# Performance work log

Measured on AMD Instinct MI355X. Metric: run time of the kernel, lower is better.

The kernel has to match this reference:

```python
import jax, jax.numpy as jnp
import numpy as np
import math

B, P, PIX, D, C = 128, 256, 256, 512, 10
MAX_STEPS, TOL, EPS = 4, 1e-3, 1e-5


def setup_inputs() -> dict:
    key = jax.random.key(0)
    ks = jax.random.split(key, 12)
    pi = math.pi
    return {
        "x": jax.random.normal(ks[0], (B, P, PIX), jnp.float32),
        "Wp": jax.random.normal(ks[1], (D, PIX), jnp.float32) * (1.0 / math.sqrt(PIX)),
        "bp": jnp.zeros((D,), jnp.float32),
        "q_rot": jax.random.uniform(ks[2], (D,), jnp.float32, -pi, pi),
        "k_rot": jax.random.uniform(ks[3], (D,), jnp.float32, -pi, pi),
        "v_rot": jax.random.uniform(ks[4], (D,), jnp.float32, -pi, pi),
        "ff_real": jax.random.normal(ks[5], (D, D), jnp.float32) * (1.0 / math.sqrt(D)),
        "ff_imag": jax.random.uniform(ks[6], (D, D), jnp.float32, -0.01, 0.01),
        "Wr": jax.random.normal(ks[7], (C, D), jnp.float32) * 0.05,
        "br": jnp.zeros((C,), jnp.float32),
        "Wi": jax.random.normal(ks[8], (C, D), jnp.float32) * 0.05,
        "bi": jnp.zeros((C,), jnp.float32),
    }


def _complex_norm(x):
    # normalize magnitude stats over last dim, preserve phase (torch.std uses ddof=1)
    mag = jnp.abs(x)
    mean_mag = jnp.mean(mag, axis=-1, keepdims=True)
    std_mag = jnp.std(mag, axis=-1, keepdims=True, ddof=1)
    norm_mag = (mag - mean_mag) / (std_mag + EPS)
    scale = jnp.tanh(norm_mag) / (mag + EPS)
    return x * scale


def _fro(z):
    return jnp.sqrt(jnp.sum(jnp.abs(z) ** 2))


def _pos_phase():
    pos = jnp.arange(P, dtype=jnp.float32)[:, None]
    dim = jnp.arange(D, dtype=jnp.float32)[None, :]
    freq = 1.0 / (10000.0 ** (dim / D))
    return pos * freq * math.pi  # (P, D)


def reference(x, Wp, bp, q_rot, k_rot, v_rot, ff_real, ff_imag, Wr, br, Wi, bi):
    mag = jnp.tanh(jnp.einsum('bpi,di->bpd', x, Wp) + bp)
    state = mag.astype(jnp.complex64) * jnp.exp(1j * _pos_phase())[None]  # (B,P,D)
    ff = (ff_real + 1j * ff_imag).astype(jnp.complex64)
    eq, ek, ev = jnp.exp(1j * q_rot), jnp.exp(1j * k_rot), jnp.exp(1j * v_rot)
    scale = 8.0 / math.sqrt(D)
    active = jnp.array(True)
    for _ in range(MAX_STEPS):  # fixed small iteration count; updates frozen after convergence
        prev = state
        q, k, v = state * eq, state * ek, state * ev
        interference = jnp.einsum('bpd,bqd->bpq', q, jnp.conj(k))
        attn = jax.nn.softmax(interference.real * scale, axis=-1)
        attn_out = jnp.einsum('bpq,bqd->bpd', attn.astype(jnp.complex64), v)
        new_state = _complex_norm((prev + attn_out) @ ff)
        diff = _fro(new_state - prev) / (_fro(new_state) + 1e-8)
        state = jnp.where(active, new_state, prev)
        active = jnp.logical_and(active, diff >= TOL)
    pooled = jnp.mean(state, axis=1)  # (B,D) complex
    logits = pooled.real @ Wr.T + br + pooled.imag @ Wi.T + bi
    return logits
```

## Files before the change

kernel.cpp:

```cpp
#include <hip/hip_runtime.h>
#include <math.h>

#define BB   128
#define PP   256
#define PIX_ 256
#define DD   512
#define CC   10
#define MTOT (BB*PP)
#define NK   1024
#define KA   2048
#define KB2  2048
#define NSLOT (MTOT/4)

static constexpr float SCALE_F = 0.35355339059327373f;
static constexpr float PI_F    = 3.14159265358979323846f;

typedef short bf16x8 __attribute__((ext_vector_type(8)));
typedef float f32x4  __attribute__((ext_vector_type(4)));
typedef unsigned short ushort8 __attribute__((ext_vector_type(8)));

__device__ __forceinline__ unsigned short f2bf(float f) {
    union { float f; unsigned u; } v; v.f = f;
    unsigned r = v.u + 0x7FFF + ((v.u >> 16) & 1);
    return (unsigned short)(r >> 16);
}
__device__ __forceinline__ float bf2f(unsigned short h) {
    union { unsigned u; float f; } v; v.u = ((unsigned)h) << 16;
    return v.f;
}

typedef __attribute__((address_space(3))) unsigned lds_u32;
typedef __attribute__((address_space(1))) const unsigned glb_u32;
__device__ __forceinline__ void gl2lds16(const unsigned short* g, short* l) {
    __builtin_amdgcn_global_load_lds((glb_u32*)g, (lds_u32*)l, 16, 0, 0);
}

__global__ void k_setup(const float* __restrict__ q_rot, const float* __restrict__ k_rot,
                        const float* __restrict__ v_rot,
                        float* __restrict__ freq, float* __restrict__ cd, float* __restrict__ sd,
                        float* __restrict__ cv, float* __restrict__ sv,
                        int* __restrict__ active) {
    int t = threadIdx.x;
    if (t < DD) {
        freq[t] = expf(-(float)t * (9.210340371976184f / 512.0f));
        float dl = q_rot[t] - k_rot[t];
        cd[t] = cosf(dl);       sd[t] = sinf(dl);
        cv[t] = cosf(v_rot[t]); sv[t] = sinf(v_rot[t]);
    }
    if (t == 0) *active = 1;
}

__global__ __launch_bounds__(256) void k_tab(const float* __restrict__ freq,
                                             float* __restrict__ Tc, float* __restrict__ Ts) {
    const int p = blockIdx.x, t = threadIdx.x;
#pragma unroll
    for (int j = 0; j < 2; j++) {
        const int d = t * 2 + j;
        float s, c; sincosf((float)p * freq[d] * PI_F, &s, &c);
        Tc[(size_t)p * DD + d] = c;
        Ts[(size_t)p * DD + d] = s;
    }
}

__global__ __launch_bounds__(256) void k_prep2(const float* __restrict__ Fr, const float* __restrict__ Fi,
                                               unsigned short* __restrict__ Bt2) {
    const int n = blockIdx.x;
    const int t = threadIdx.x;
    unsigned short* row = Bt2 + (size_t)n * KB2;
#pragma unroll
    for (int j4 = 0; j4 < 4; j4++) {
        const int j = j4 * 256 + t;
        float v;
        if (n < 512) v = (j < 512) ? Fr[(size_t)j * DD + n] : -Fi[(size_t)(j - 512) * DD + n];
        else         v = (j < 512) ? Fi[(size_t)j * DD + (n - 512)] : Fr[(size_t)(j - 512) * DD + (n - 512)];
        const unsigned short hi = f2bf(v);
        row[j] = hi;
        row[NK + j] = f2bf(v - bf2f(hi));
    }
}

#define SCAT4(TILE, V4) do { TILE[lk+0][lrow]=(V4).x; TILE[lk+1][lrow]=(V4).y; \
                             TILE[lk+2][lrow]=(V4).z; TILE[lk+3][lrow]=(V4).w; } while(0)

__global__ __launch_bounds__(256) void k_init(const float* __restrict__ x,
        const float* __restrict__ Wp, const float* __restrict__ bp,
        const float* __restrict__ Tc, const float* __restrict__ Ts,
        float* __restrict__ Sr, float* __restrict__ Si) {
    __shared__ float As[16][68];
    __shared__ float Bs[16][68];
    const int bm = blockIdx.y * 64, bn = blockIdx.x * 64;
    const int t = threadIdx.x, tx = t & 15, ty = t >> 4;
    const int lrow = t >> 2, lk = (t & 3) * 4;
    float acc[4][4] = {};
    for (int k0 = 0; k0 < PIX_; k0 += 16) {
        const float4 a4 = *(const float4*)(x  + (size_t)(bm + lrow) * PIX_ + k0 + lk);
        const float4 b4 = *(const float4*)(Wp + (size_t)(bn + lrow) * PIX_ + k0 + lk);
        __syncthreads();
        SCAT4(As, a4);
        SCAT4(Bs, b4);
        __syncthreads();
#pragma unroll
        for (int kk = 0; kk < 16; ++kk) {
            const float4 av = *(const float4*)&As[kk][ty * 4];
            const float4 bv = *(const float4*)&Bs[kk][tx * 4];
            const float a[4] = {av.x, av.y, av.z, av.w};
            const float b[4] = {bv.x, bv.y, bv.z, bv.w};
#pragma unroll
            for (int i = 0; i < 4; i++)
#pragma unroll
                for (int j = 0; j < 4; j++) acc[i][j] = fmaf(a[i], b[j], acc[i][j]);
        }
    }
#pragma unroll
    for (int i = 0; i < 4; i++) {
        const int m = bm + ty * 4 + i;
        const int p = m & 255;
        const float4 c4 = *(const float4*)(Tc + (size_t)p * DD + bn + tx * 4);
        const float4 s4 = *(const float4*)(Ts + (size_t)p * DD + bn + tx * 4);
        const float cphv[4] = {c4.x, c4.y, c4.z, c4.w};
        const float sphv[4] = {s4.x, s4.y, s4.z, s4.w};
        float4 vr, vi;
        float* pvr = (float*)&vr; float* pvi = (float*)&vi;
#pragma unroll
        for (int j = 0; j < 4; j++) {
            const int d = bn + tx * 4 + j;
            const float mg = tanhf(acc[i][j] + bp[d]);
            pvr[j] = mg * cphv[j]; pvi[j] = mg * sphv[j];
        }
        *(float4*)(Sr + (size_t)m * DD + bn + tx * 4) = vr;
        *(float4*)(Si + (size_t)m * DD + bn + tx * 4) = vi;
    }
}

__global__ __launch_bounds__(256) void k_xy(const float* __restrict__ Sr, const float* __restrict__ Si,
        const float* __restrict__ cd, const float* __restrict__ sd,
        unsigned short* X, unsigned short* Y,
        const int* __restrict__ active) {
    if (*active == 0) return;
    const int r = blockIdx.x, t = threadIdx.x;
    const size_t base = (size_t)r * DD + 2 * t;
    const float2 s_r = *(const float2*)(Sr + base);
    const float2 s_i = *(const float2*)(Si + base);
    const float2 c2  = *(const float2*)(cd + 2 * t);
    const float2 s2  = *(const float2*)(sd + 2 * t);
    unsigned short* xr = X + (size_t)r * KA;
    unsigned short* yr = Y + (size_t)r * KA;
    const float srv[2] = {s_r.x, s_r.y}, siv[2] = {s_i.x, s_i.y};
    const float cv_[2] = {c2.x, c2.y},  sv_[2] = {s2.x, s2.y};
    ushort2 xh_r, xh_i, xl_r, xl_i, yh_r, yh_i, yl_r, yl_i;
    unsigned short* o[8] = {(unsigned short*)&xh_r, (unsigned short*)&xh_i,
                            (unsigned short*)&xl_r, (unsigned short*)&xl_i,
                            (unsigned short*)&yh_r, (unsigned short*)&yh_i,
                            (unsigned short*)&yl_r, (unsigned short*)&yl_i};
#pragma unroll
    for (int e = 0; e < 2; e++) {
        const unsigned short hr = f2bf(srv[e]);
        const unsigned short hi_ = f2bf(siv[e]);
        o[0][e] = hr;  o[2][e] = f2bf(srv[e] - bf2f(hr));
        o[1][e] = hi_; o[3][e] = f2bf(siv[e] - bf2f(hi_));
        const float krr = srv[e] * cv_[e] + siv[e] * sv_[e];
        const float kri = siv[e] * cv_[e] - srv[e] * sv_[e];
        const unsigned short yh1 = f2bf(krr);
        const unsigned short yh2 = f2bf(kri);
        o[4][e] = yh1; o[6][e] = f2bf(krr - bf2f(yh1));
        o[5][e] = yh2; o[7][e] = f2bf(kri - bf2f(yh2));
    }
    *(ushort2*)(xr + 2 * t)        = xh_r;
    *(ushort2*)(xr + 512 + 2 * t)  = xh_i;
    *(ushort2*)(xr + 1024 + 2 * t) = xl_r;
    *(ushort2*)(xr + 1536 + 2 * t) = xl_i;
    *(ushort2*)(yr + 2 * t)        = yh_r;
    *(ushort2*)(yr + 512 + 2 * t)  = yh_i;
    *(ushort2*)(yr + 1024 + 2 * t) = yl_r;
    *(ushort2*)(yr + 1536 + 2 * t) = yl_i;
}

__global__ __launch_bounds__(256) void k_score_sm(const unsigned short* __restrict__ X,
        const unsigned short* __restrict__ Y,
        unsigned short* __restrict__ Asp, const int* __restrict__ active) {
    if (*active == 0) return;
    __shared__ short SM[20480];
    short* XH = SM;
    short* XL = SM + 2048;
    short* YH = SM + 4096;
    short* YL = SM + 12288;
    const int t = threadIdx.x;
    const int w = t >> 6, L = t & 63;
    const int lane15 = L & 15, quad = L >> 4;
    const int nsm = (int)gridDim.x >> 2;
    const int s   = (int)blockIdx.x & (nsm - 1);
    const int rt  = (int)blockIdx.x / nsm;
    const int bm = s * 256 + rt * 64;
    const int yb = s * 256;
    const int gr = t >> 2, ch = (t & 3) * 8;
    short* XHw = XH + w * 512;
    short* XLw = XL + w * 512;
    short* YHw = YH + w * 512;
    short* YLw = YL + w * 512;
    f32x4 acc[16] = {};
    for (int k0 = 0; k0 < 1024; k0 += 32) {
        __syncthreads();
        gl2lds16(X + (size_t)(bm + gr) * KA + k0 + ch,        XHw);
        gl2lds16(X + (size_t)(bm + gr) * KA + 1024 + k0 + ch, XLw);
#pragma unroll
        for (int ss = 0; ss < 4; ss++) {
            gl2lds16(Y + (size_t)(yb + ss * 64 + gr) * KA + k0 + ch,        YHw + ss * 2048);
            gl2lds16(Y + (size_t)(yb + ss * 64 + gr) * KA + 1024 + k0 + ch, YLw + ss * 2048);
        }
        __syncthreads();
        const bf16x8 xh = *(const bf16x8*)(XH + (w * 16 + lane15) * 32 + quad * 8);
        const bf16x8 xl = *(const bf16x8*)(XL + (w * 16 + lane15) * 32 + quad * 8);
#pragma unroll
        for (int tc = 0; tc < 16; tc++) {
            const bf16x8 yh = *(const bf16x8*)(YH + (tc * 16 + lane15) * 32 + quad * 8);
            acc[tc] = __builtin_amdgcn_mfma_f32_16x16x32_bf16(xh, yh, acc[tc], 0, 0, 0);
            acc[tc] = __builtin_amdgcn_mfma_f32_16x16x32_bf16(xl, yh, acc[tc], 0, 0, 0);
            const bf16x8 yl = *(const bf16x8*)(YL + (tc * 16 + lane15) * 32 + quad * 8);
            acc[tc] = __builtin_amdgcn_mfma_f32_16x16x32_bf16(xh, yl, acc[tc], 0, 0, 0);
        }
    }
#pragma unroll
    for (int tc = 0; tc < 16; tc++) acc[tc] *= SCALE_F;
#pragma unroll
    for (int r = 0; r < 4; r++) {
        float mx = acc[0][r];
#pragma unroll
        for (int tc = 1; tc < 16; tc++) mx = fmaxf(mx, acc[tc][r]);
#pragma unroll
        for (int off = 8; off; off >>= 1) mx = fmaxf(mx, __shfl_xor(mx, off, 64));
        float sum = 0.f;
#pragma unroll
        for (int tc = 0; tc < 16; tc++) { acc[tc][r] = __expf(acc[tc][r] - mx); sum += acc[tc][r]; }
#pragma unroll
        for (int off = 8; off; off >>= 1) sum += __shfl_xor(sum, off, 64);
        const float inv = 1.0f / sum;
#pragma unroll
        for (int tc = 0; tc < 16; tc++) acc[tc][r] *= inv;
    }
    __syncthreads();
#pragma unroll
    for (int h = 0; h < 2; h++) {
        if ((w >> 1) == h) {
#pragma unroll
            for (int r = 0; r < 4; r++) {
                const int lr = (w & 1) * 16 + quad * 4 + r;
#pragma unroll
                for (int tc = 0; tc < 16; tc++) {
                    const float p = acc[tc][r];
                    const unsigned short hi = f2bf(p);
                    SM[lr * 520 + tc * 16 + lane15] = (short)hi;
                    SM[lr * 520 + 256 + tc * 16 + lane15] = (short)f2bf(p - bf2f(hi));
                }
            }
        }
        __syncthreads();
        unsigned short* dst = Asp + (size_t)(bm + h * 32) * 512;
#pragma unroll
        for (int k = 0; k < 8; k++) {
            const int c = t + 256 * k;
            const int row = c >> 6, off = (c & 63) * 8;
            *(ushort8*)(dst + (size_t)c * 8) = *(const ushort8*)&SM[row * 520 + off];
        }
        __syncthreads();
    }
}

__global__ __launch_bounds__(256) void k_attnout_mfma(const unsigned short* __restrict__ Asp,
        const unsigned short* __restrict__ X,
        const float* __restrict__ Sr, const float* __restrict__ Si,
        const float* __restrict__ cv, const float* __restrict__ sv,
        unsigned short* __restrict__ A2, const int* __restrict__ active) {
    if (*active == 0) return;
    __shared__ short AhT[128][32];
    __shared__ short AlT[128][32];
    __shared__ short BH[128][40];
    __shared__ short BL[128][40];
    const int t = threadIdx.x;
    const int w = t >> 6, L = t & 63;
    const int lane15 = L & 15, quad = L >> 4;
    const int bm = blockIdx.x * 128;
    const int bn = blockIdx.y * 64;
    const int sample = blockIdx.x >> 1;
    const int gr = t >> 2, ch = (t & 3) * 8;
    short* AhW0 = &AhT[0][0] + w * 512;
    short* AhW1 = AhW0 + 64 * 32;
    short* AlW0 = &AlT[0][0] + w * 512;
    short* AlW1 = AlW0 + 64 * 32;
    const int nn = t & 127, kh = t >> 7;
    const unsigned short* Bsrc = X + (size_t)sample * PP * KA
                               + ((nn < 64) ? (bn + nn) : (512 + bn + nn - 64));
    f32x4 acc[2][8] = {};
    for (int q0 = 0; q0 < PP; q0 += 32) {
        __syncthreads();
        gl2lds16(Asp + (size_t)(bm + gr) * 512      + q0 + ch,       AhW0);
        gl2lds16(Asp + (size_t)(bm + 64 + gr) * 512 + q0 + ch,       AhW1);
        gl2lds16(Asp + (size_t)(bm + gr) * 512      + 256 + q0 + ch, AlW0);
        gl2lds16(Asp + (size_t)(bm + 64 + gr) * 512 + 256 + q0 + ch, AlW1);
#pragma unroll
        for (int kg = 0; kg < 2; kg++) {
            const int qb = kh * 16 + kg * 8;
            bf16x8 hh, ll;
#pragma unroll
            for (int j = 0; j < 8; j++) {
                const size_t o = (size_t)(q0 + qb + j) * KA;
                hh[j] = (short)Bsrc[o];
                ll[j] = (short)Bsrc[o + 1024];
            }
            *(bf16x8*)&BH[nn][qb] = hh;
            *(bf16x8*)&BL[nn][qb] = ll;
        }
        __syncthreads();
        bf16x8 bh[8];
#pragma unroll
        for (int tc = 0; tc < 8; tc++)
            bh[tc] = *(const bf16x8*)&BH[tc * 16 + lane15][quad * 8];
        bf16x8 afh[2];
#pragma unroll
        for (int tr = 0; tr < 2; tr++) {
            afh[tr] = *(const bf16x8*)&AhT[w * 32 + tr * 16 + lane15][quad * 8];
            const bf16x8 afl = *(const bf16x8*)&AlT[w * 32 + tr * 16 + lane15][quad * 8];
#pragma unroll
            for (int tc = 0; tc < 8; tc++)
                acc[tr][tc] = __builtin_amdgcn_mfma_f32_16x16x32_bf16(afh[tr], bh[tc], acc[tr][tc], 0, 0, 0);
#pragma unroll
            for (int tc = 0; tc < 8; tc++)
                acc[tr][tc] = __builtin_amdgcn_mfma_f32_16x16x32_bf16(afl, bh[tc], acc[tr][tc], 0, 0, 0);
        }
#pragma unroll
        for (int tc = 0; tc < 8; tc++) {
            const bf16x8 bl = *(const bf16x8*)&BL[tc * 16 + lane15][quad * 8];
            acc[0][tc] = __builtin_amdgcn_mfma_f32_16x16x32_bf16(afh[0], bl, acc[0][tc], 0, 0, 0);
            acc[1][tc] = __builtin_amdgcn_mfma_f32_16x16x32_bf16(afh[1], bl, acc[1][tc], 0, 0, 0);
        }
    }
#pragma unroll
    for (int tr = 0; tr < 2; tr++) {
#pragma unroll
        for (int tc = 0; tc < 4; tc++) {
            const int d = bn + tc * 16 + lane15;
            const float cvd = cv[d], svd = sv[d];
#pragma unroll
            for (int r = 0; r < 4; r++) {
                const int m = bm + w * 32 + tr * 16 + quad * 4 + r;
                const float wr = acc[tr][tc][r];
                const float wi = acc[tr][tc + 4][r];
                const float tr_ = Sr[(size_t)m * DD + d] + (wr * cvd - wi * svd);
                const float ti_ = Si[(size_t)m * DD + d] + (wr * svd + wi * cvd);
                const unsigned short rh = f2bf(tr_);
                const unsigned short ih = f2bf(ti_);
                unsigned short* arow = A2 + (size_t)m * KA;
                arow[d]        = rh;
                arow[512 + d]  = ih;
                arow[1024 + d] = f2bf(tr_ - bf2f(rh));
                arow[1536 + d] = f2bf(ti_ - bf2f(ih));
            }
        }
    }
}

__global__ __launch_bounds__(256) void k_ff_mfma2(const unsigned short* __restrict__ A2,
        const unsigned short* __restrict__ Bt2,
        float* __restrict__ U, const int* __restrict__ active) {
    if (*active == 0) return;
    __shared__ short AH[128][32], AL[128][32];
    __shared__ short BH[128][32], BL[128][32];
    const int t = threadIdx.x;
    const int w = t >> 6, L = t & 63;
    const int lane15 = L & 15, quad = L >> 4;
    const int bm = blockIdx.x * 128, bn = blockIdx.y * 128;
    const int gr = t >> 2, ch = (t & 3) * 8;
    short* AHw = &AH[0][0] + w * 512;
    short* ALw = &AL[0][0] + w * 512;
    short* BHw = &BH[0][0] + w * 512;
    short* BLw = &BL[0][0] + w * 512;
    f32x4 acc[2][8] = {};
    for (int k0 = 0; k0 < 1024; k0 += 32) {
        __syncthreads();
        gl2lds16(A2  + (size_t)(bm + gr) * KA       + k0 + ch,        AHw);
        gl2lds16(A2  + (size_t)(bm + 64 + gr) * KA  + k0 + ch,        AHw + 64 * 32);
        gl2lds16(A2  + (size_t)(bm + gr) * KA       + 1024 + k0 + ch, ALw);
        gl2lds16(A2  + (size_t)(bm + 64 + gr) * KA  + 1024 + k0 + ch, ALw + 64 * 32);
        gl2lds16(Bt2 + (size_t)(bn + gr) * KB2      + k0 + ch,        BHw);
        gl2lds16(Bt2 + (size_t)(bn + 64 + gr) * KB2 + k0 + ch,        BHw + 64 * 32);
        gl2lds16(Bt2 + (size_t)(bn + gr) * KB2      + 1024 + k0 + ch, BLw);
        gl2lds16(Bt2 + (size_t)(bn + 64 + gr) * KB2 + 1024 + k0 + ch, BLw + 64 * 32);
        __syncthreads();
        bf16x8 ah[2], al[2];
#pragma unroll
        for (int tr = 0; tr < 2; tr++) {
            ah[tr] = *(const bf16x8*)&AH[w * 32 + tr * 16 + lane15][quad * 8];
            al[tr] = *(const bf16x8*)&AL[w * 32 + tr * 16 + lane15][quad * 8];
        }
#pragma unroll
        for (int tc = 0; tc < 8; tc++) {
            const bf16x8 bh = *(const bf16x8*)&BH[tc * 16 + lane15][quad * 8];
            acc[0][tc] = __builtin_amdgcn_mfma_f32_16x16x32_bf16(ah[0], bh, acc[0][tc], 0, 0, 0);
            acc[1][tc] = __builtin_amdgcn_mfma_f32_16x16x32_bf16(ah[1], bh, acc[1][tc], 0, 0, 0);
            acc[0][tc] = __builtin_amdgcn_mfma_f32_16x16x32_bf16(al[0], bh, acc[0][tc], 0, 0, 0);
            acc[1][tc] = __builtin_amdgcn_mfma_f32_16x16x32_bf16(al[1], bh, acc[1][tc], 0, 0, 0);
            const bf16x8 bl = *(const bf16x8*)&BL[tc * 16 + lane15][quad * 8];
            acc[0][tc] = __builtin_amdgcn_mfma_f32_16x16x32_bf16(ah[0], bl, acc[0][tc], 0, 0, 0);
            acc[1][tc] = __builtin_amdgcn_mfma_f32_16x16x32_bf16(ah[1], bl, acc[1][tc], 0, 0, 0);
        }
    }
#pragma unroll
    for (int tr = 0; tr < 2; tr++)
#pragma unroll
        for (int tc = 0; tc < 8; tc++) {
            const int n = bn + tc * 16 + lane15;
            const int mbase = bm + w * 32 + tr * 16 + quad * 4;
#pragma unroll
            for (int r = 0; r < 4; r++)
                U[(size_t)(mbase + r) * NK + n] = acc[tr][tc][r];
        }
}

__global__ __launch_bounds__(256) void k_norm(const float* U,
        float* __restrict__ Sr, float* __restrict__ Si,
        float* __restrict__ part,
        unsigned short* X, unsigned short* Y,
        const float* __restrict__ cd, const float* __restrict__ sd,
        const int wxy, const int* __restrict__ active) {
    if (*active == 0) return;
    __shared__ float red[8];
    const int t = threadIdx.x, rt = t >> 6, L = t & 63;
    const int row = blockIdx.x * 4 + rt;
    const size_t ub = (size_t)row * NK;
    const size_t base = (size_t)row * DD;
    const float4 ur0 = *(const float4*)(U + ub + 4 * L);
    const float4 ur1 = *(const float4*)(U + ub + 256 + 4 * L);
    const float4 ui0 = *(const float4*)(U + ub + 512 + 4 * L);
    const float4 ui1 = *(const float4*)(U + ub + 768 + 4 * L);
    const float4 pr0 = *(const float4*)(Sr + base + 4 * L);
    const float4 pr1 = *(const float4*)(Sr + base + 256 + 4 * L);
    const float4 pi0 = *(const float4*)(Si + base + 4 * L);
    const float4 pi1 = *(const float4*)(Si + base + 256 + 4 * L);
    const float urr[8] = {ur0.x, ur0.y, ur0.z, ur0.w, ur1.x, ur1.y, ur1.z, ur1.w};
    const float uii[8] = {ui0.x, ui0.y, ui0.z, ui0.w, ui1.x, ui1.y, ui1.z, ui1.w};
    float mg[8], msum = 0.f;
#pragma unroll
    for (int e = 0; e < 8; e++) {
        mg[e] = sqrtf(urr[e] * urr[e] + uii[e] * uii[e]);
        msum += mg[e];
    }
#pragma unroll
    for (int off = 32; off; off >>= 1) msum += __shfl_xor(msum, off, 64);
    const float mean = msum * (1.0f / 512.0f);
    float vs = 0.f;
#pragma unroll
    for (int e = 0; e < 8; e++) { const float d = mg[e] - mean; vs += d * d; }
#pragma unroll
    for (int off = 32; off; off >>= 1) vs += __shfl_xor(vs, off, 64);
    const float istd = 1.0f / (sqrtf(vs * (1.0f / 511.0f)) + 1e-5f);
    float nr[8], ni[8];
#pragma unroll
    for (int e = 0; e < 8; e++) {
        const float sc = tanhf((mg[e] - mean) * istd) / (mg[e] + 1e-5f);
        nr[e] = urr[e] * sc; ni[e] = uii[e] * sc;
    }
    const float prr[8] = {pr0.x, pr0.y, pr0.z, pr0.w, pr1.x, pr1.y, pr1.z, pr1.w};
    const float pii[8] = {pi0.x, pi0.y, pi0.z, pi0.w, pi1.x, pi1.y, pi1.z, pi1.w};
    float dd = 0.f, nn = 0.f;
#pragma unroll
    for (int e = 0; e < 8; e++) {
        const float dr = nr[e] - prr[e], di = ni[e] - pii[e];
        dd += dr * dr + di * di;
        nn += nr[e] * nr[e] + ni[e] * ni[e];
    }
    *(float4*)(Sr + base + 4 * L)       = make_float4(nr[0], nr[1], nr[2], nr[3]);
    *(float4*)(Sr + base + 256 + 4 * L) = make_float4(nr[4], nr[5], nr[6], nr[7]);
    *(float4*)(Si + base + 4 * L)       = make_float4(ni[0], ni[1], ni[2], ni[3]);
    *(float4*)(Si + base + 256 + 4 * L) = make_float4(ni[4], ni[5], ni[6], ni[7]);
    if (wxy) {
        unsigned short* xr = X + (size_t)row * KA;
        unsigned short* yr = Y + (size_t)row * KA;
        const float4 c0 = *(const float4*)(cd + 4 * L);
        const float4 c1 = *(const float4*)(cd + 256 + 4 * L);
        const float4 s0 = *(const float4*)(sd + 4 * L);
        const float4 s1 = *(const float4*)(sd + 256 + 4 * L);
        const float cdv[8] = {c0.x, c0.y, c0.z, c0.w, c1.x, c1.y, c1.z, c1.w};
        const float sdv[8] = {s0.x, s0.y, s0.z, s0.w, s1.x, s1.y, s1.z, s1.w};
        ushort4 xhr[2], xhi[2], xlr[2], xli[2], yhr[2], yhi[2], ylr[2], yli[2];
#pragma unroll
        for (int e = 0; e < 8; e++) {
            const int g = e >> 2, j = e & 3;
            const unsigned short hr = f2bf(nr[e]);
            const unsigned short hi_ = f2bf(ni[e]);
            ((unsigned short*)&xhr[g])[j] = hr;
            ((unsigned short*)&xlr[g])[j] = f2bf(nr[e] - bf2f(hr));
            ((unsigned short*)&xhi[g])[j] = hi_;
            ((unsigned short*)&xli[g])[j] = f2bf(ni[e] - bf2f(hi_));
            const float krr = nr[e] * cdv[e] + ni[e] * sdv[e];
            const float kri = ni[e] * cdv[e] - nr[e] * sdv[e];
            const unsigned short k1 = f2bf(krr);
            const unsigned short k2 = f2bf(kri);
            ((unsigned short*)&yhr[g])[j] = k1;
            ((unsigned short*)&ylr[g])[j] = f2bf(krr - bf2f(k1));
            ((unsigned short*)&yhi[g])[j] = k2;
            ((unsigned short*)&yli[g])[j] = f2bf(kri - bf2f(k2));
        }
        *(ushort4*)(xr + 4 * L)        = xhr[0]; *(ushort4*)(xr + 256 + 4 * L)  = xhr[1];
        *(ushort4*)(xr + 512 + 4 * L)  = xhi[0]; *(ushort4*)(xr + 768 + 4 * L)  = xhi[1];
        *(ushort4*)(xr + 1024 + 4 * L) = xlr[0]; *(ushort4*)(xr + 1280 + 4 * L) = xlr[1];
        *(ushort4*)(xr + 1536 + 4 * L) = xli[0]; *(ushort4*)(xr + 1792 + 4 * L) = xli[1];
        *(ushort4*)(yr + 4 * L)        = yhr[0]; *(ushort4*)(yr + 256 + 4 * L)  = yhr[1];
        *(ushort4*)(yr + 512 + 4 * L)  = yhi[0]; *(ushort4*)(yr + 768 + 4 * L)  = yhi[1];
        *(ushort4*)(yr + 1024 + 4 * L) = ylr[0]; *(ushort4*)(yr + 1280 + 4 * L) = ylr[1];
        *(ushort4*)(yr + 1536 + 4 * L) = yli[0]; *(ushort4*)(yr + 1792 + 4 * L) = yli[1];
    }
#pragma unroll
    for (int off = 32; off; off >>= 1) {
        dd += __shfl_xor(dd, off, 64);
        nn += __shfl_xor(nn, off, 64);
    }
    if (L == 0) { red[rt] = dd; red[4 + rt] = nn; }
    __syncthreads();
    if (t == 0)
        *(float2*)(part + 2 * blockIdx.x) =
            make_float2(red[0] + red[1] + red[2] + red[3],
                        red[4] + red[5] + red[6] + red[7]);
}

__global__ __launch_bounds__(256) void k_flag(const float* __restrict__ part, int* __restrict__ active) {
    __shared__ float red[8];
    const int t = threadIdx.x, rt = t >> 6, L = t & 63;
    float dd = 0.f, nn = 0.f;
    for (int i = t; i < NSLOT; i += 256) {
        const float2 p = *(const float2*)(part + 2 * i);
        dd += p.x; nn += p.y;
    }
#pragma unroll
    for (int off = 32; off; off >>= 1) {
        dd += __shfl_xor(dd, off, 64);
        nn += __shfl_xor(nn, off, 64);
    }
    if (L == 0) { red[rt] = dd; red[4 + rt] = nn; }
    __syncthreads();
    if (t == 0) {
        const float d = red[0] + red[1] + red[2] + red[3];
        const float n = red[4] + red[5] + red[6] + red[7];
        const float diff = sqrtf(d) / (sqrtf(n) + 1e-8f);
        const int a = *active;
        *active = (a && (diff >= 1e-3f)) ? 1 : 0;
    }
}

__global__ __launch_bounds__(256) void k_pool(const float* __restrict__ Sr, const float* __restrict__ Si,
        float* __restrict__ Pr, float* __restrict__ Pi) {
    const int gid = blockIdx.x * 256 + threadIdx.x;
    const int b = gid >> 9, d = gid & 511;
    const size_t base = (size_t)b * PP * DD + d;
    float sr = 0.f, si = 0.f;
    for (int p = 0; p < PP; p++) {
        sr += Sr[base + (size_t)p * DD];
        si += Si[base + (size_t)p * DD];
    }
    Pr[gid] = sr * (1.0f / 256.0f);
    Pi[gid] = si * (1.0f / 256.0f);
}

__global__ __launch_bounds__(64) void k_logits(const float* __restrict__ Pr, const float* __restrict__ Pi,
        const float* __restrict__ Wr, const float* __restrict__ br,
        const float* __restrict__ Wi, const float* __restrict__ bi,
        float* __restrict__ out) {
    const int b = blockIdx.x;
    const int lane = threadIdx.x;
    for (int c = 0; c < CC; c++) {
        float acc = 0.f;
#pragma unroll
        for (int k = 0; k < 8; k++) {
            const int d = lane + 64 * k;
            acc += Pr[b * DD + d] * Wr[c * DD + d] + Pi[b * DD + d] * Wi[c * DD + d];
        }
#pragma unroll
        for (int off = 32; off; off >>= 1) acc += __shfl_xor(acc, off, 64);
        if (lane == 0) out[b * CC + c] = acc + br[c] + bi[c];
    }
}

extern "C" void kernel_launch(void* const* d_in, const int* in_sizes, int n_in,
                              void* d_out, int out_size, void* d_ws, size_t ws_size,
                              hipStream_t stream) {
    const float* x     = (const float*)d_in[0];
    const float* Wp    = (const float*)d_in[1];
    const float* bp    = (const float*)d_in[2];
    const float* q_rot = (const float*)d_in[3];
    const float* k_rot = (const float*)d_in[4];
    const float* v_rot = (const float*)d_in[5];
    const float* ffr   = (const float*)d_in[6];
    const float* ffi   = (const float*)d_in[7];
    const float* Wr    = (const float*)d_in[8];
    const float* br    = (const float*)d_in[9];
    const float* Wi    = (const float*)d_in[10];
    const float* bi    = (const float*)d_in[11];
    float* out = (float*)d_out;

    float* ws = (float*)d_ws;
    const size_t plane = (size_t)MTOT * DD;
    const size_t sline = (size_t)PP * DD;

    float* freq = ws;
    float* cd   = freq + DD;
    float* sd   = cd + DD;
    float* cv   = sd + DD;
    float* sv   = cv + DD;
    int*   active = (int*)(sv + DD);
    float* Pr = ws + 4096;
    float* Pi = Pr + (size_t)BB * DD;
    float* part = Pi + (size_t)BB * DD;
    float* Sr = part + 2 * NSLOT;
    float* Si = Sr + plane;
    unsigned short* Bt2 = (unsigned short*)(Si + plane);
    float* Tc = (float*)(Bt2 + (size_t)NK * KB2);
    float* Ts = Tc + (size_t)PP * DD;
    float* chunkbase = Si + plane + (size_t)NK * 3072 / 2;

    const size_t fixed_f = (4096 + 2 * (size_t)BB * DD + 2 * NSLOT) + 2 * plane + (size_t)NK * 3072 / 2;
    const size_t perC_f = (size_t)PP * NK * 2 + (size_t)PP * 256;

    int C = BB;
    while (C > 1 && (fixed_f + (size_t)C * perC_f) * 4ull > ws_size) C >>= 1;
    const int fullXY = (C == BB);

    float* U = chunkbase;
    unsigned short* X  = (unsigned short*)chunkbase;
    float* Yf = chunkbase + (size_t)C * PP * NK;
    unsigned short* Y  = (unsigned short*)Yf;
    unsigned short* A2 = Y;
    unsigned short* Asp = (unsigned short*)(Yf + (size_t)C * PP * NK);

    k_setup<<<1, 512, 0, stream>>>(q_rot, k_rot, v_rot, freq, cd, sd, cv, sv, active);
    k_tab<<<PP, 256, 0, stream>>>(freq, Tc, Ts);
    k_prep2<<<NK, 256, 0, stream>>>(ffr, ffi, Bt2);
    k_init<<<dim3(DD / 64, MTOT / 64), 256, 0, stream>>>(x, Wp, bp, Tc, Ts, Sr, Si);

    for (int it = 0; it < 4; ++it) {
        for (int c0 = 0; c0 < BB; c0 += C) {
            float* Sr_c = Sr + (size_t)c0 * sline;
            float* Si_c = Si + (size_t)c0 * sline;
            float* part_c = part + (size_t)c0 * (PP / 4) * 2;
            if (!fullXY || it == 0)
                k_xy<<<C * PP, 256, 0, stream>>>(Sr_c, Si_c, cd, sd, X, Y, active);
            k_score_sm<<<C * 4, 256, 0, stream>>>(X, Y, Asp, active);
            k_attnout_mfma<<<dim3(C * 2, 8), 256, 0, stream>>>(Asp, X, Sr_c, Si_c, cv, sv, A2, active);
            k_ff_mfma2<<<dim3(C * 2, NK / 128), 256, 0, stream>>>(A2, Bt2, U, active);
            k_norm<<<C * (PP / 4), 256, 0, stream>>>(U, Sr_c, Si_c, part_c, X, Y, cd, sd, fullXY, active);
        }
        k_flag<<<1, 256, 0, stream>>>(part, active);
    }

    k_pool<<<BB * DD / 256, 256, 0, stream>>>(Sr, Si, Pr, Pi);
    k_logits<<<BB, 64, 0, stream>>>(Pr, Pi, Wr, br, Wi, bi, out);
}
```

Measured before the change: 3.003 ms.

## Drop fp32 state planes; keep state only as packed hi/lo bf16 X

When the workspace is large enough, the fp32 Sr/Si state planes are removed and the state is carried only as packed hi+lo bf16 in X. k_init writes X and Y directly, so the first k_xy pass is skipped. k_attnout, k_norm and k_pool rebuild fp32 values from hi+lo, which cuts fp32 state reads and writes per iteration. The state is now held to roughly bf16x2 precision instead of full fp32, and the old chunked path stays as a fallback.

```diff
diff --git a/kernel.cpp b/kernel.cpp
--- a/kernel.cpp
+++ b/kernel.cpp
@@ -85,7 +85,10 @@
 __global__ __launch_bounds__(256) void k_init(const float* __restrict__ x,
         const float* __restrict__ Wp, const float* __restrict__ bp,
         const float* __restrict__ Tc, const float* __restrict__ Ts,
-        float* __restrict__ Sr, float* __restrict__ Si) {
+        float* Sr, float* Si,
+        unsigned short* X, unsigned short* Y,
+        const float* __restrict__ cd, const float* __restrict__ sd,
+        const int packed) {
     __shared__ float As[16][68];
     __shared__ float Bs[16][68];
     const int bm = blockIdx.y * 64, bn = blockIdx.x * 64;
@@ -111,6 +114,10 @@
                 for (int j = 0; j < 4; j++) acc[i][j] = fmaf(a[i], b[j], acc[i][j]);
         }
     }
+    const float4 cd4 = *(const float4*)(cd + bn + tx * 4);
+    const float4 sd4 = *(const float4*)(sd + bn + tx * 4);
+    const float cdv[4] = {cd4.x, cd4.y, cd4.z, cd4.w};
+    const float sdv[4] = {sd4.x, sd4.y, sd4.z, sd4.w};
 #pragma unroll
     for (int i = 0; i < 4; i++) {
         const int m = bm + ty * 4 + i;
@@ -119,16 +126,46 @@
         const float4 s4 = *(const float4*)(Ts + (size_t)p * DD + bn + tx * 4);
         const float cphv[4] = {c4.x, c4.y, c4.z, c4.w};
         const float sphv[4] = {s4.x, s4.y, s4.z, s4.w};
-        float4 vr, vi;
-        float* pvr = (float*)&vr; float* pvi = (float*)&vi;
+        float srv[4], siv[4];
 #pragma unroll
         for (int j = 0; j < 4; j++) {
             const int d = bn + tx * 4 + j;
             const float mg = tanhf(acc[i][j] + bp[d]);
-            pvr[j] = mg * cphv[j]; pvi[j] = mg * sphv[j];
-        }
-        *(float4*)(Sr + (size_t)m * DD + bn + tx * 4) = vr;
-        *(float4*)(Si + (size_t)m * DD + bn + tx * 4) = vi;
+            srv[j] = mg * cphv[j]; siv[j] = mg * sphv[j];
+        }
+        if (packed) {
+            ushort4 xhr, xhi, xlr, xli, yhr, yhi, ylr, yli;
+            unsigned short* po[8] = {(unsigned short*)&xhr, (unsigned short*)&xhi,
+                                     (unsigned short*)&xlr, (unsigned short*)&xli,
+                                     (unsigned short*)&yhr, (unsigned short*)&yhi,
+                                     (unsigned short*)&ylr, (unsigned short*)&yli};
+#pragma unroll
+            for (int j = 0; j < 4; j++) {
+                const unsigned short hr = f2bf(srv[j]);
+                const unsigned short hi_ = f2bf(siv[j]);
+                po[0][j] = hr;  po[2][j] = f2bf(srv[j] - bf2f(hr));
+                po[1][j] = hi_; po[3][j] = f2bf(siv[j] - bf2f(hi_));
+                const float krr = srv[j] * cdv[j] + siv[j] * sdv[j];
+                const float kri = siv[j] * cdv[j] - srv[j] * sdv[j];
+                const unsigned short y1 = f2bf(krr);
+                const unsigned short y2 = f2bf(kri);
+                po[4][j] = y1; po[6][j] = f2bf(krr - bf2f(y1));
+                po[5][j] = y2; po[7][j] = f2bf(kri - bf2f(y2));
+            }
+            unsigned short* xr = X + (size_t)m * KA + bn + tx * 4;
+            unsigned short* yr = Y + (size_t)m * KA + bn + tx * 4;
+            *(ushort4*)(xr)        = xhr; *(ushort4*)(xr + 512)  = xhi;
+            *(ushort4*)(xr + 1024) = xlr; *(ushort4*)(xr + 1536) = xli;
+            *(ushort4*)(yr)        = yhr; *(ushort4*)(yr + 512)  = yhi;
+            *(ushort4*)(yr + 1024) = ylr; *(ushort4*)(yr + 1536) = yli;
+        } else {
+            float4 vr, vi;
+            float* pvr = (float*)&vr; float* pvi = (float*)&vi;
+#pragma unroll
+            for (int j = 0; j < 4; j++) { pvr[j] = srv[j]; pvi[j] = siv[j]; }
+            *(float4*)(Sr + (size_t)m * DD + bn + tx * 4) = vr;
+            *(float4*)(Si + (size_t)m * DD + bn + tx * 4) = vi;
+        }
     }
 }
 
@@ -267,7 +304,6 @@
 
 __global__ __launch_bounds__(256) void k_attnout_mfma(const unsigned short* __restrict__ Asp,
         const unsigned short* __restrict__ X,
-        const float* __restrict__ Sr, const float* __restrict__ Si,
         const float* __restrict__ cv, const float* __restrict__ sv,
         unsigned short* __restrict__ A2, const int* __restrict__ active) {
     if (*active == 0) return;
@@ -342,10 +378,13 @@
 #pragma unroll
             for (int r = 0; r < 4; r++) {
                 const int m = bm + w * 32 + tr * 16 + quad * 4 + r;
+                const unsigned short* xrow = X + (size_t)m * KA + d;
+                const float pvr = bf2f(xrow[0])   + bf2f(xrow[1024]);
+                const float pvi = bf2f(xrow[512]) + bf2f(xrow[1536]);
                 const float wr = acc[tr][tc][r];
                 const float wi = acc[tr][tc + 4][r];
-                const float tr_ = Sr[(size_t)m * DD + d] + (wr * cvd - wi * svd);
-                const float ti_ = Si[(size_t)m * DD + d] + (wr * svd + wi * cvd);
+                const float tr_ = pvr + (wr * cvd - wi * svd);
+                const float ti_ = pvi + (wr * svd + wi * cvd);
                 const unsigned short rh = f2bf(tr_);
                 const unsigned short ih = f2bf(ti_);
                 unsigned short* arow = A2 + (size_t)m * KA;
@@ -416,11 +455,11 @@
 }
 
 __global__ __launch_bounds__(256) void k_norm(const float* U,
-        float* __restrict__ Sr, float* __restrict__ Si,
+        float* Sr, float* Si,
         float* __restrict__ part,
         unsigned short* X, unsigned short* Y,
         const float* __restrict__ cd, const float* __restrict__ sd,
-        const int wxy, const int* __restrict__ active) {
+        const int mode, const int* __restrict__ active) {
     if (*active == 0) return;
     __shared__ float red[8];
     const int t = threadIdx.x, rt = t >> 6, L = t & 63;
@@ -431,10 +470,37 @@
     const float4 ur1 = *(const float4*)(U + ub + 256 + 4 * L);
     const float4 ui0 = *(const float4*)(U + ub + 512 + 4 * L);
     const float4 ui1 = *(const float4*)(U + ub + 768 + 4 * L);
-    const float4 pr0 = *(const float4*)(Sr + base + 4 * L);
-    const float4 pr1 = *(const float4*)(Sr + base + 256 + 4 * L);
-    const float4 pi0 = *(const float4*)(Si + base + 4 * L);
-    const float4 pi1 = *(const float4*)(Si + base + 256 + 4 * L);
+    float prr[8], pii[8];
+    unsigned short* xr = X + (size_t)row * KA;
+    if (mode == 2) {
+        const ushort4 hr0 = *(const ushort4*)(xr + 4 * L);
+        const ushort4 hr1 = *(const ushort4*)(xr + 256 + 4 * L);
+        const ushort4 hi0 = *(const ushort4*)(xr + 512 + 4 * L);
+        const ushort4 hi1 = *(const ushort4*)(xr + 768 + 4 * L);
+        const ushort4 lr0 = *(const ushort4*)(xr + 1024 + 4 * L);
+        const ushort4 lr1 = *(const ushort4*)(xr + 1280 + 4 * L);
+        const ushort4 li0 = *(const ushort4*)(xr + 1536 + 4 * L);
+        const ushort4 li1 = *(const ushort4*)(xr + 1792 + 4 * L);
+        const unsigned short* hr[2] = {(const unsigned short*)&hr0, (const unsigned short*)&hr1};
+        const unsigned short* hi[2] = {(const unsigned short*)&hi0, (const unsigned short*)&hi1};
+        const unsigned short* lr[2] = {(const unsigned short*)&lr0, (const unsigned short*)&lr1};
+        const unsigned short* li[2] = {(const unsigned short*)&li0, (const unsigned short*)&li1};
+#pragma unroll
+        for (int e = 0; e < 8; e++) {
+            const int g = e >> 2, j = e & 3;
+            prr[e] = bf2f(hr[g][j]) + bf2f(lr[g][j]);
+            pii[e] = bf2f(hi[g][j]) + bf2f(li[g][j]);
+        }
+    } else {
+        const float4 pr0 = *(const float4*)(Sr + base + 4 * L);
+        const float4 pr1 = *(const float4*)(Sr + base + 256 + 4 * L);
+        const float4 pi0 = *(const float4*)(Si + base + 4 * L);
+        const float4 pi1 = *(const float4*)(Si + base + 256 + 4 * L);
+        prr[0] = pr0.x; prr[1] = pr0.y; prr[2] = pr0.z; prr[3] = pr0.w;
+        prr[4] = pr1.x; prr[5] = pr1.y; prr[6] = pr1.z; prr[7] = pr1.w;
+        pii[0] = pi0.x; pii[1] = pi0.y; pii[2] = pi0.z; pii[3] = pi0.w;
+        pii[4] = pi1.x; pii[5] = pi1.y; pii[6] = pi1.z; pii[7] = pi1.w;
+    }
     const float urr[8] = {ur0.x, ur0.y, ur0.z, ur0.w, ur1.x, ur1.y, ur1.z, ur1.w};
     const float uii[8] = {ui0.x, ui0.y, ui0.z, ui0.w, ui1.x, ui1.y, ui1.z, ui1.w};
     float mg[8], msum = 0.f;
@@ -458,8 +524,6 @@
         const float sc = tanhf((mg[e] - mean) * istd) / (mg[e] + 1e-5f);
         nr[e] = urr[e] * sc; ni[e] = uii[e] * sc;
     }
-    const float prr[8] = {pr0.x, pr0.y, pr0.z, pr0.w, pr1.x, pr1.y, pr1.z, pr1.w};
-    const float pii[8] = {pi0.x, pi0.y, pi0.z, pi0.w, pi1.x, pi1.y, pi1.z, pi1.w};
     float dd = 0.f, nn = 0.f;
 #pragma unroll
     for (int e = 0; e < 8; e++) {
@@ -467,12 +531,13 @@
         dd += dr * dr + di * di;
         nn += nr[e] * nr[e] + ni[e] * ni[e];
     }
-    *(float4*)(Sr + base + 4 * L)       = make_float4(nr[0], nr[1], nr[2], nr[3]);
-    *(float4*)(Sr + base + 256 + 4 * L) = make_float4(nr[4], nr[5], nr[6], nr[7]);
-    *(float4*)(Si + base + 4 * L)       = make_float4(ni[0], ni[1], ni[2], ni[3]);
-    *(float4*)(Si + base + 256 + 4 * L) = make_float4(ni[4], ni[5], ni[6], ni[7]);
-    if (wxy) {
-        unsigned short* xr = X + (size_t)row * KA;
+    if (mode != 2) {
+        *(float4*)(Sr + base + 4 * L)       = make_float4(nr[0], nr[1], nr[2], nr[3]);
+        *(float4*)(Sr + base + 256 + 4 * L) = make_float4(nr[4], nr[5], nr[6], nr[7]);
+        *(float4*)(Si + base + 4 * L)       = make_float4(ni[0], ni[1], ni[2], ni[3]);
+        *(float4*)(Si + base + 256 + 4 * L) = make_float4(ni[4], ni[5], ni[6], ni[7]);
+    }
+    if (mode >= 1) {
         unsigned short* yr = Y + (size_t)row * KA;
         const float4 c0 = *(const float4*)(cd + 4 * L);
         const float4 c1 = *(const float4*)(cd + 256 + 4 * L);
@@ -484,10 +549,10 @@
 #pragma unroll
         for (int e = 0; e < 8; e++) {
             const int g = e >> 2, j = e & 3;
-            const unsigned short hr = f2bf(nr[e]);
+            const unsigned short hr_ = f2bf(nr[e]);
             const unsigned short hi_ = f2bf(ni[e]);
-            ((unsigned short*)&xhr[g])[j] = hr;
-            ((unsigned short*)&xlr[g])[j] = f2bf(nr[e] - bf2f(hr));
+            ((unsigned short*)&xhr[g])[j] = hr_;
+            ((unsigned short*)&xlr[g])[j] = f2bf(nr[e] - bf2f(hr_));
             ((unsigned short*)&xhi[g])[j] = hi_;
             ((unsigned short*)&xli[g])[j] = f2bf(ni[e] - bf2f(hi_));
             const float krr = nr[e] * cdv[e] + ni[e] * sdv[e];
@@ -546,14 +611,24 @@
 }
 
 __global__ __launch_bounds__(256) void k_pool(const float* __restrict__ Sr, const float* __restrict__ Si,
-        float* __restrict__ Pr, float* __restrict__ Pi) {
+        const unsigned short* __restrict__ X,
+        float* __restrict__ Pr, float* __restrict__ Pi, const int packed) {
     const int gid = blockIdx.x * 256 + threadIdx.x;
     const int b = gid >> 9, d = gid & 511;
-    const size_t base = (size_t)b * PP * DD + d;
     float sr = 0.f, si = 0.f;
-    for (int p = 0; p < PP; p++) {
-        sr += Sr[base + (size_t)p * DD];
-        si += Si[base + (size_t)p * DD];
+    if (packed) {
+        const unsigned short* xb = X + ((size_t)b * PP) * KA + d;
+        for (int p = 0; p < PP; p++) {
+            const unsigned short* xr = xb + (size_t)p * KA;
+            sr += bf2f(xr[0])   + bf2f(xr[1024]);
+            si += bf2f(xr[512]) + bf2f(xr[1536]);
+        }
+    } else {
+        const size_t base = (size_t)b * PP * DD + d;
+        for (int p = 0; p < PP; p++) {
+            sr += Sr[base + (size_t)p * DD];
+            si += Si[base + (size_t)p * DD];
+        }
     }
     Pr[gid] = sr * (1.0f / 256.0f);
     Pi[gid] = si * (1.0f / 256.0f);
@@ -608,47 +683,83 @@
     float* Pr = ws + 4096;
     float* Pi = Pr + (size_t)BB * DD;
     float* part = Pi + (size_t)BB * DD;
-    float* Sr = part + 2 * NSLOT;
-    float* Si = Sr + plane;
-    unsigned short* Bt2 = (unsigned short*)(Si + plane);
-    float* Tc = (float*)(Bt2 + (size_t)NK * KB2);
-    float* Ts = Tc + (size_t)PP * DD;
-    float* chunkbase = Si + plane + (size_t)NK * 3072 / 2;
-
-    const size_t fixed_f = (4096 + 2 * (size_t)BB * DD + 2 * NSLOT) + 2 * plane + (size_t)NK * 3072 / 2;
-    const size_t perC_f = (size_t)PP * NK * 2 + (size_t)PP * 256;
-
-    int C = BB;
-    while (C > 1 && (fixed_f + (size_t)C * perC_f) * 4ull > ws_size) C >>= 1;
-    const int fullXY = (C == BB);
-
-    float* U = chunkbase;
-    unsigned short* X  = (unsigned short*)chunkbase;
-    float* Yf = chunkbase + (size_t)C * PP * NK;
-    unsigned short* Y  = (unsigned short*)Yf;
-    unsigned short* A2 = Y;
-    unsigned short* Asp = (unsigned short*)(Yf + (size_t)C * PP * NK);
+
+    const size_t headf = 151552;
+    const size_t btf   = (size_t)NK * KB2 / 2;
+    const size_t tabf  = 2 * (size_t)PP * DD;
+    const size_t xf    = (size_t)MTOT * KA / 2;
+    const size_t packed_f = headf + btf + tabf + 3 * xf;
+    const int packed = ((packed_f * 4ull) <= ws_size);
 
     k_setup<<<1, 512, 0, stream>>>(q_rot, k_rot, v_rot, freq, cd, sd, cv, sv, active);
-    k_tab<<<PP, 256, 0, stream>>>(freq, Tc, Ts);
-    k_prep2<<<NK, 256, 0, stream>>>(ffr, ffi, Bt2);
-    k_init<<<dim3(DD / 64, MTOT / 64), 256, 0, stream>>>(x, Wp, bp, Tc, Ts, Sr, Si);
-
-    for (int it = 0; it < 4; ++it) {
-        for (int c0 = 0; c0 < BB; c0 += C) {
-            float* Sr_c = Sr + (size_t)c0 * sline;
-            float* Si_c = Si + (size_t)c0 * sline;
-            float* part_c = part + (size_t)c0 * (PP / 4) * 2;
-            if (!fullXY || it == 0)
-                k_xy<<<C * PP, 256, 0, stream>>>(Sr_c, Si_c, cd, sd, X, Y, active);
-            k_score_sm<<<C * 4, 256, 0, stream>>>(X, Y, Asp, active);
-            k_attnout_mfma<<<dim3(C * 2, 8), 256, 0, stream>>>(Asp, X, Sr_c, Si_c, cv, sv, A2, active);
-            k_ff_mfma2<<<dim3(C * 2, NK / 128), 256, 0, stream>>>(A2, Bt2, U, active);
-            k_norm<<<C * (PP / 4), 256, 0, stream>>>(U, Sr_c, Si_c, part_c, X, Y, cd, sd, fullXY, active);
-        }
-        k_flag<<<1, 256, 0, stream>>>(part, active);
-    }
-
-    k_pool<<<BB * DD / 256, 256, 0, stream>>>(Sr, Si, Pr, Pi);
+
+    if (packed) {
+        unsigned short* Bt2 = (unsigned short*)(ws + headf);
+        float* Tc = (float*)(Bt2 + (size_t)NK * KB2);
+        float* Ts = Tc + (size_t)PP * DD;
+        unsigned short* X = (unsigned short*)(Ts + (size_t)PP * DD);
+        unsigned short* Y = X + (size_t)MTOT * KA;
+        unsigned short* Asp = Y + (size_t)MTOT * KA;
+        unsigned short* A2 = Y;
+        float* U = (float*)Asp;
+
+        k_tab<<<PP, 256, 0, stream>>>(freq, Tc, Ts);
+        k_prep2<<<NK, 256, 0, stream>>>(ffr, ffi, Bt2);
+        k_init<<<dim3(DD / 64, MTOT / 64), 256, 0, stream>>>(x, Wp, bp, Tc, Ts,
+                nullptr, nullptr, X, Y, cd, sd, 1);
+
+        for (int it = 0; it < 4; ++it) {
+            k_score_sm<<<BB * 4, 256, 0, stream>>>(X, Y, Asp, active);
+            k_attnout_mfma<<<dim3(BB * 2, 8), 256, 0, stream>>>(Asp, X, cv, sv, A2, active);
+            k_ff_mfma2<<<dim3(BB * 2, NK / 128), 256, 0, stream>>>(A2, Bt2, U, active);
+            k_norm<<<BB * (PP / 4), 256, 0, stream>>>(U, nullptr, nullptr, part, X, Y, cd, sd, 2, active);
+            k_flag<<<1, 256, 0, stream>>>(part, active);
+        }
+        k_pool<<<BB * DD / 256, 256, 0, stream>>>(nullptr, nullptr, X, Pr, Pi, 1);
+    } else {
+        float* Sr = part + 2 * NSLOT;
+        float* Si = Sr + plane;
+        unsigned short* Bt2 = (unsigned short*)(Si + plane);
+        float* Tc = (float*)(Bt2 + (size_t)NK * KB2);
+        float* Ts = Tc + (size_t)PP * DD;
+        float* chunkbase = Si + plane + (size_t)NK * 3072 / 2;
+
+        const size_t fixed_f = (4096 + 2 * (size_t)BB * DD + 2 * NSLOT) + 2 * plane + (size_t)NK * 3072 / 2;
+        const size_t perC_f = (size_t)PP * NK * 2 + (size_t)PP * 256;
+
+        int C = BB;
+        while (C > 1 && (fixed_f + (size_t)C * perC_f) * 4ull > ws_size) C >>= 1;
+        const int fullXY = (C == BB);
+
+        float* U = chunkbase;
+        unsigned short* X  = (unsigned short*)chunkbase;
+        float* Yf = chunkbase + (size_t)C * PP * NK;
+        unsigned short* Y  = (unsigned short*)Yf;
+        unsigned short* A2 = Y;
+        unsigned short* Asp = (unsigned short*)(Yf + (size_t)C * PP * NK);
+
+        k_tab<<<PP, 256, 0, stream>>>(freq, Tc, Ts);
+        k_prep2<<<NK, 256, 0, stream>>>(ffr, ffi, Bt2);
+        k_init<<<dim3(DD / 64, MTOT / 64), 256, 0, stream>>>(x, Wp, bp, Tc, Ts,
+                Sr, Si, nullptr, nullptr, cd, sd, 0);
+
+        for (int it = 0; it < 4; ++it) {
+            for (int c0 = 0; c0 < BB; c0 += C) {
+                float* Sr_c = Sr + (size_t)c0 * sline;
+                float* Si_c = Si + (size_t)c0 * sline;
+                float* part_c = part + (size_t)c0 * (PP / 4) * 2;
+                if (!fullXY || it == 0)
+                    k_xy<<<C * PP, 256, 0, stream>>>(Sr_c, Si_c, cd, sd, X, Y, active);
+                k_score_sm<<<C * 4, 256, 0, stream>>>(X, Y, Asp, active);
+                k_attnout_mfma<<<dim3(C * 2, 8), 256, 0, stream>>>(Asp, X, cv, sv, A2, active);
+                k_ff_mfma2<<<dim3(C * 2, NK / 128), 256, 0, stream>>>(A2, Bt2, U, active);
+                k_norm<<<C * (PP / 4), 256, 0, stream>>>(U, Sr_c, Si_c, part_c, X, Y, cd, sd,
+                                                         fullXY ? 1 : 0, active);
+            }
+            k_flag<<<1, 256, 0, stream>>>(part, active);
+        }
+        k_pool<<<BB * DD / 256, 256, 0, stream>>>(Sr, Si, nullptr, Pr, Pi, 0);
+    }
+
     k_logits<<<BB, 64, 0, stream>>>(Pr, Pi, Wr, br, Wi, bi, out);
 }
```

Measured after the change: 3.031 ms (median of 3 runs). Within noise of the previous version (+0.9%).
